# Kernel tuning notes

Hardware: AMD Instinct MI355X
Metric: run time of the kernel (lower is better)

Reference implementation:

```python
import jax, jax.numpy as jnp
import numpy as np

DIM = 1024
NUM_HEADS = 16
HEAD_DIM = DIM // NUM_HEADS


def apply_rotary_embed(x, thetas):
    # x: (..., seq, d), thetas: (seq, d) broadcast over leading dims
    x1, x2 = jnp.split(x, 2, axis=-1)
    x_rot = jnp.concatenate([-x2, x1], axis=-1)
    return x * jnp.cos(thetas) + x_rot * jnp.sin(thetas)


def setup_inputs() -> dict:
    key = jax.random.key(0)
    ks = jax.random.split(key, 8)
    B, Nx, Nc = 4, 1024, 2048
    x = jax.random.normal(ks[0], (B, Nx, DIM), dtype=jnp.float32)
    c = jax.random.normal(ks[1], (B, Nc, DIM), dtype=jnp.float32)
    x_pos_embed = jax.random.normal(ks[2], (Nx, HEAD_DIM), dtype=jnp.float32)
    c_pos_embed = jax.random.normal(ks[3], (Nc, HEAD_DIM), dtype=jnp.float32)
    s = 1.0 / np.sqrt(DIM)
    Wq = jax.random.normal(ks[4], (DIM, DIM), dtype=jnp.float32) * s
    Wkv = jax.random.normal(ks[5], (DIM, 2 * DIM), dtype=jnp.float32) * s
    Wproj = jax.random.normal(ks[6], (DIM, DIM), dtype=jnp.float32) * s
    bproj = jnp.zeros((DIM,), dtype=jnp.float32)
    return {"x": x, "c": c, "x_pos_embed": x_pos_embed, "c_pos_embed": c_pos_embed,
            "Wq": Wq, "Wkv": Wkv, "Wproj": Wproj, "bproj": bproj}


def reference(x, c, x_pos_embed, c_pos_embed, Wq, Wkv, Wproj, bproj):
    B, Nx, D = x.shape
    Nc = c.shape[1]
    H, hd = NUM_HEADS, HEAD_DIM
    # Q projection -> (B, H, Nx, hd)
    q = (x @ Wq).reshape(B, Nx, H, hd).transpose(0, 2, 1, 3)
    q = apply_rotary_embed(q, x_pos_embed)
    # KV projection -> k, v each (B, H, Nc, hd)
    kv = (c @ Wkv).reshape(B, Nc, 2, H, hd).transpose(2, 0, 3, 1, 4)
    k, v = kv[0], kv[1]
    k = apply_rotary_embed(k, c_pos_embed)
    # scaled dot-product attention (dropout p=0 -> identity)
    scale = 1.0 / np.sqrt(hd).astype(np.float32)
    attn = jnp.einsum('bhqd,bhkd->bhqk', q, k) * scale
    attn = jax.nn.softmax(attn, axis=-1)
    out = jnp.einsum('bhqk,bhkd->bhqd', attn, v)
    out = out.transpose(0, 2, 1, 3).reshape(B, Nx, D)
    return out @ Wproj + bproj
```

## Files before the change

kernel.cpp:

```cpp
#include <hip/hip_runtime.h>
#include <math.h>

#define DIMC  1024
#define NHEAD 16
#define HD    64
#define NB    4
#define NX    1024
#define NC    2048
#define KD    1024

typedef _Float16 half_t;
typedef __attribute__((ext_vector_type(8))) _Float16 h8;
typedef __attribute__((ext_vector_type(4))) _Float16 h4;
typedef __attribute__((ext_vector_type(2))) __fp16 fp16x2;
typedef __attribute__((ext_vector_type(4))) float f32x4;

#define QSCALE 0.1803368801111244f
#define NEGM  -8.656170245333781f

__device__ __forceinline__ void gload_lds16(const half_t* g, half_t* l) {
    __builtin_amdgcn_global_load_lds(
        (__attribute__((address_space(1))) void*)(g),
        (__attribute__((address_space(3))) void*)(l), 16, 0, 0);
}

__device__ __forceinline__ void wtile(const float* __restrict__ W,
                                      half_t* __restrict__ Wt, int N, int IMG,
                                      int bx, int by, int t)
{
    __shared__ half_t T[64][72];
    const int k0 = by * 64, n0 = bx * 64;
    const int kr = t >> 2, c0 = (t & 3) << 4;
    const float* src = W + (size_t)(k0 + kr) * N + n0 + c0;
#pragma unroll
    for (int j = 0; j < 16; j += 4) {
        float4 v = *(const float4*)(src + j);
        T[c0 + j + 0][kr] = (half_t)v.x;
        T[c0 + j + 1][kr] = (half_t)v.y;
        T[c0 + j + 2][kr] = (half_t)v.z;
        T[c0 + j + 3][kr] = (half_t)v.w;
    }
    __syncthreads();
    const int nr = t >> 2, kc = (t & 3) << 4;
    if (!IMG) {
        half_t* dst = Wt + (size_t)(n0 + nr) * KD + k0 + kc;
        *(int4*)dst       = *(const int4*)&T[nr][kc];
        *(int4*)(dst + 8) = *(const int4*)&T[nr][kc + 8];
    } else {
        const int n = n0 + nr;
        const int ntile = n >> 8, rr = n & 255;
        const int s0 = kc >> 3;
        half_t* base = Wt + ((size_t)(ntile * 16 + by) * 256 + rr) * 64;
        *(int4*)(base + ((s0 ^ (rr & 7)) << 3))       = *(const int4*)&T[nr][kc];
        *(int4*)(base + (((s0 + 1) ^ (rr & 7)) << 3)) = *(const int4*)&T[nr][kc + 8];
    }
}

__global__ __launch_bounds__(256) void prep(
    const float* __restrict__ x, half_t* __restrict__ xh,
    const float* __restrict__ c, half_t* __restrict__ ch,
    const float* __restrict__ xpe, const float* __restrict__ cpe,
    float* __restrict__ xct, float* __restrict__ xst,
    float* __restrict__ cct, float* __restrict__ cst,
    const float* __restrict__ Wq,  half_t* __restrict__ Wqt,
    const float* __restrict__ Wkv, half_t* __restrict__ Wkt,
    const float* __restrict__ Wp,  half_t* __restrict__ Wpt)
{
    const int bid = blockIdx.x, t = threadIdx.x;
    if (bid < 1024) {
        if (bid < 256)      wtile(Wq,  Wqt, DIMC, 0,     bid & 15,         bid >> 4,         t);
        else if (bid < 768) wtile(Wkv, Wkt, 2 * DIMC, 1, (bid - 256) & 31, (bid - 256) >> 5, t);
        else                wtile(Wp,  Wpt, DIMC, 0,     (bid - 768) & 15, (bid - 768) >> 4, t);
    } else if (bid < 7168) {
        const int nx = NB * NX * DIMC;
        const int i = ((bid - 1024) * 256 + t) * 8;
        const float* s;
        h8 o;
        if (i < nx) {
            s = x + i;
            float4 a = *(const float4*)(s);
            float4 b = *(const float4*)(s + 4);
            o[0] = (half_t)a.x; o[1] = (half_t)a.y; o[2] = (half_t)a.z; o[3] = (half_t)a.w;
            o[4] = (half_t)b.x; o[5] = (half_t)b.y; o[6] = (half_t)b.z; o[7] = (half_t)b.w;
            *(h8*)(xh + i) = o;
        } else {
            const int j = i - nx;
            s = c + j;
            float4 a = *(const float4*)(s);
            float4 b = *(const float4*)(s + 4);
            o[0] = (half_t)a.x; o[1] = (half_t)a.y; o[2] = (half_t)a.z; o[3] = (half_t)a.w;
            o[4] = (half_t)b.x; o[5] = (half_t)b.y; o[6] = (half_t)b.z; o[7] = (half_t)b.w;
            const int R = j >> 10, k = j & 1023;
            const int mt = R >> 8, r = R & 255, kt = k >> 6, sl = (k & 63) >> 3;
            *(h8*)(ch + ((size_t)(mt * 16 + kt) * 256 + r) * 64 + ((sl ^ (r & 7)) << 3)) = o;
        }
    } else {
        const int i = (bid - 7168) * 256 + t;
        if (i < NX * HD) {
            const float th = xpe[i];
            xct[i] = cosf(th); xst[i] = sinf(th);
        } else {
            const int j = i - NX * HD;
            const float th = cpe[j];
            cct[j] = cosf(th); cst[j] = sinf(th);
        }
    }
}

template <int MODE, int BN>
__global__ __launch_bounds__(256) void hgemm(
    const half_t* __restrict__ Ag, const half_t* __restrict__ Bt,
    const float* __restrict__ ct, const float* __restrict__ st,
    const float* __restrict__ bias,
    void* __restrict__ out0, void* __restrict__ out1)
{
    constexpr int MI = (BN == 128) ? 4 : 2;
    constexpr int BLOADS = BN / 32;
    __shared__ half_t As[2][8192];
    __shared__ half_t Bs[2][BN * 64];

    const int tid = threadIdx.x;
    const int w = tid >> 6, lane = tid & 63;
    const int lr = lane & 15, lg = lane >> 4;
    const int wrOff = (BN == 128) ? (w >> 1) * 64 : w * 32;
    const int wcOff = (BN == 128) ? (w & 1) * 64 : 0;

    int lin = (int)blockIdx.x;
    lin = (lin & 7) * ((int)gridDim.x >> 3) + (lin >> 3);
    const int m0 = (lin >> 4) * 128, n0 = (lin & 15) * BN;

    f32x4 acc[MI][4];
#pragma unroll
    for (int i = 0; i < MI; ++i)
#pragma unroll
        for (int j = 0; j < 4; ++j) acc[i][j] = f32x4{0.f, 0.f, 0.f, 0.f};

    size_t gA[4], gB[BLOADS];
    int loff[4];
#pragma unroll
    for (int c = 0; c < 4; ++c) {
        const int L = c * 4096 + w * 1024 + lane * 16;
        const int row = L >> 7;
        const int ss = ((L >> 4) & 7) ^ (row & 7);
        gA[c] = (size_t)(m0 + row) * KD + ss * 8;
        if (c < BLOADS) gB[c] = (size_t)(n0 + row) * KD + ss * 8;
        loff[c] = c * 2048 + w * 512;
    }

#define HSTAGE(buf, kk) do {                                               \
        _Pragma("unroll")                                                  \
        for (int c = 0; c < 4; ++c) {                                      \
            gload_lds16(Ag + gA[c] + (kk) * 64, &As[buf][loff[c]]);        \
            if (c < BLOADS) gload_lds16(Bt + gB[c] + (kk) * 64, &Bs[buf][loff[c]]); \
        }                                                                  \
    } while (0)

    HSTAGE(0, 0);
    asm volatile("s_waitcnt vmcnt(0)" ::: "memory");
    __builtin_amdgcn_s_barrier();
    __builtin_amdgcn_sched_barrier(0);

    for (int k = 0; k < KD / 64; ++k) {
        const int cb = k & 1;
        if (k + 1 < KD / 64) {
            HSTAGE(cb ^ 1, k + 1);
            if constexpr (BLOADS == 4)
                asm volatile("s_waitcnt vmcnt(8)" ::: "memory");
            else
                asm volatile("s_waitcnt vmcnt(6)" ::: "memory");
        } else {
            asm volatile("s_waitcnt vmcnt(0)" ::: "memory");
        }
        __builtin_amdgcn_s_barrier();
        __builtin_amdgcn_sched_barrier(0);

        __builtin_amdgcn_s_setprio(1);
#pragma unroll
        for (int kc = 0; kc < 2; ++kc) {
            h8 af[MI], bf[4];
#pragma unroll
            for (int mi = 0; mi < MI; ++mi) {
                const int r = wrOff + mi * 16 + lr;
                af[mi] = *(const h8*)&As[cb][r * 64 + (((kc * 4 + lg) ^ (r & 7)) << 3)];
            }
#pragma unroll
            for (int ni = 0; ni < 4; ++ni) {
                const int r = wcOff + ni * 16 + lr;
                bf[ni] = *(const h8*)&Bs[cb][r * 64 + (((kc * 4 + lg) ^ (r & 7)) << 3)];
            }
#pragma unroll
            for (int mi = 0; mi < MI; ++mi)
#pragma unroll
                for (int ni = 0; ni < 4; ++ni)
                    acc[mi][ni] = __builtin_amdgcn_mfma_f32_16x16x32_f16(
                        af[mi], bf[ni], acc[mi][ni], 0, 0, 0);
        }
        __builtin_amdgcn_s_setprio(0);

        __builtin_amdgcn_s_barrier();
        __builtin_amdgcn_sched_barrier(0);
    }
#undef HSTAGE

    if (MODE == 2) {
        float* o = (float*)out0;
#pragma unroll
        for (int ni = 0; ni < 4; ++ni) {
            const int col = n0 + ni * 16 + lr;
            const float bv = bias[col];
#pragma unroll
            for (int mi = 0; mi < MI; ++mi)
#pragma unroll
                for (int r = 0; r < 4; ++r) {
                    const int row = m0 + wrOff + mi * 16 + lg * 4 + r;
                    o[(size_t)row * DIMC + col] = acc[mi][ni][r] + bv;
                }
        }
        return;
    }

    if (MODE == 0) {
        half_t* Qw = (half_t*)out0;
        const int h = n0 >> 6;
#pragma unroll
        for (int mi = 0; mi < MI; ++mi)
#pragma unroll
            for (int r = 0; r < 4; ++r) {
                const int row = m0 + wrOff + mi * 16 + lg * 4 + r;
                const int bb = row >> 10, nn = row & (NX - 1);
                const float* cr = ct + nn * HD;
                const float* sr = st + nn * HD;
                half_t* op = Qw + (((size_t)(bb * NHEAD + h)) * NX + nn) * HD;
#pragma unroll
                for (int ni = 0; ni < 4; ++ni) {
                    const int d = ni * 16 + lr;
                    const float val = acc[mi][ni][r];
                    const float pv  = acc[mi][ni ^ 2][r];
                    op[d] = (half_t)((val * cr[d] + (ni < 2 ? -pv : pv) * sr[d]) * QSCALE);
                }
            }
    }
}

__global__ __launch_bounds__(512, 2) void hgemm_kv(
    const half_t* __restrict__ Aimg, const half_t* __restrict__ Bimg,
    const float* __restrict__ ct, const float* __restrict__ st,
    half_t* __restrict__ Kw, half_t* __restrict__ Vw)
{
    __shared__ half_t lds[65536];

    const int tid = threadIdx.x;
    const int w = tid >> 6, lane = tid & 63;
    const int lr = lane & 15, lg = lane >> 4;
    const int wr = w >> 2, wc = w & 3;
    const int wrOff = wr * 128, wcOff = wc * 64;

    int lin = (int)blockIdx.x;
    lin = (lin & 7) * 32 + (lin >> 3);
    const int mt = lin >> 3, nt = lin & 7;
    const int m0 = mt * 256, n0 = nt * 256;

    const half_t* Ablk = Aimg + (size_t)mt * 262144;
    const half_t* Bblk = Bimg + (size_t)nt * 262144;
    const int so2 = w * 512 + lane * 8;

    f32x4 acc[8][4];
#pragma unroll
    for (int i = 0; i < 8; ++i)
#pragma unroll
        for (int j = 0; j < 4; ++j) acc[i][j] = f32x4{0.f, 0.f, 0.f, 0.f};
    h8 af[2][2];
    h8 bf[4][2];

#define ISSUEH(SRC, DSTOFF) do {                                     \
        gload_lds16((SRC) + so2,        &lds[(DSTOFF) + w * 512]);   \
        gload_lds16((SRC) + 4096 + so2, &lds[(DSTOFF) + 4096 + w * 512]); \
    } while (0)

#define PHASE(MI0, AOFF, BOFF, READBF, STG, GATE) do {               \
        _Pragma("unroll")                                            \
        for (int kc = 0; kc < 2; ++kc)                               \
        _Pragma("unroll")                                            \
        for (int d = 0; d < 2; ++d) {                                \
            const int r_ = wrOff + ((MI0) + d) * 16 + lr;            \
            af[d][kc] = *(const h8*)&lds[(AOFF) + r_ * 64 + (((kc * 4 + lg) ^ (r_ & 7)) << 3)]; \
        }                                                            \
        if (READBF) {                                                \
            _Pragma("unroll")                                        \
            for (int ni = 0; ni < 4; ++ni)                           \
            _Pragma("unroll")                                        \
            for (int kc = 0; kc < 2; ++kc) {                         \
                const int rb = wcOff + ni * 16 + lr;                 \
                bf[ni][kc] = *(const h8*)&lds[(BOFF) + rb * 64 + (((kc * 4 + lg) ^ (rb & 7)) << 3)]; \
            }                                                        \
        }                                                            \
        STG;                                                         \
        __builtin_amdgcn_sched_barrier(0);                           \
        __builtin_amdgcn_s_barrier();                                \
        __builtin_amdgcn_s_setprio(1);                               \
        _Pragma("unroll")                                            \
        for (int d = 0; d < 2; ++d)                                  \
        _Pragma("unroll")                                            \
        for (int ni = 0; ni < 4; ++ni)                               \
        _Pragma("unroll")                                            \
        for (int kc = 0; kc < 2; ++kc)                               \
            acc[(MI0) + d][ni] = __builtin_amdgcn_mfma_f32_16x16x32_f16( \
                af[d][kc], bf[ni][kc], acc[(MI0) + d][ni], 0, 0, 0); \
        __builtin_amdgcn_s_setprio(0);                               \
        GATE;                                                        \
        __builtin_amdgcn_s_barrier();                                \
    } while (0)

#define GATE4 asm volatile("s_waitcnt vmcnt(4)" ::: "memory")
#define GATE0 asm volatile("s_waitcnt vmcnt(0)" ::: "memory")
#define NOG   ((void)0)

    ISSUEH(Ablk, 0);          ISSUEH(Ablk + 8192, 8192);
    ISSUEH(Bblk, 32768);      ISSUEH(Bblk + 8192, 32768 + 8192);
    __builtin_amdgcn_sched_barrier(0);
    ISSUEH(Bblk + 16384, 49152); ISSUEH(Bblk + 16384 + 8192, 49152 + 8192);
    asm volatile("s_waitcnt vmcnt(4)" ::: "memory");
    __builtin_amdgcn_s_barrier();

    for (int i = 0; i < 7; ++i) {
        const half_t* An1 = Ablk + (size_t)(2 * i + 1) * 16384;
        const half_t* An2 = Ablk + (size_t)(2 * i + 2) * 16384;
        const half_t* Bn2 = Bblk + (size_t)(2 * i + 2) * 16384;
        const half_t* Bn3 = Bblk + (size_t)(2 * i + 3) * 16384;
        PHASE(0, 0,     32768, true,  ISSUEH(An1, 16384),               NOG);
        PHASE(2, 0,     32768, false, ISSUEH(An1 + 8192, 16384 + 8192), NOG);
        PHASE(4, 0,     32768, false, ISSUEH(Bn2, 32768),               NOG);
        PHASE(6, 0,     32768, false, ISSUEH(Bn2 + 8192, 32768 + 8192), GATE4);
        PHASE(0, 16384, 49152, true,  ISSUEH(An2, 0),                   NOG);
        PHASE(2, 16384, 49152, false, ISSUEH(An2 + 8192, 8192),         NOG);
        PHASE(4, 16384, 49152, false, ISSUEH(Bn3, 49152),               NOG);
        PHASE(6, 16384, 49152, false, ISSUEH(Bn3 + 8192, 49152 + 8192), GATE4);
    }
    {
        const half_t* A15 = Ablk + (size_t)15 * 16384;
        PHASE(0, 0,     32768, true,  ISSUEH(A15, 16384),               NOG);
        PHASE(2, 0,     32768, false, ISSUEH(A15 + 8192, 16384 + 8192), NOG);
        PHASE(4, 0,     32768, false, NOG,                              NOG);
        PHASE(6, 0,     32768, false, NOG,                              GATE0);
        PHASE(0, 16384, 49152, true,  NOG,                              NOG);
        PHASE(2, 16384, 49152, false, NOG,                              NOG);
        PHASE(4, 16384, 49152, false, NOG,                              NOG);
        PHASE(6, 16384, 49152, false, NOG,                              NOG);
    }
#undef PHASE
#undef ISSUEH
#undef GATE4
#undef GATE0
#undef NOG

    const bool isK = (n0 < DIMC);
    const int h = ((n0 & (DIMC - 1)) >> 6) + wc;
#pragma unroll
    for (int mi = 0; mi < 8; ++mi)
#pragma unroll
        for (int r = 0; r < 4; ++r) {
            const int row = m0 + wrOff + mi * 16 + lg * 4 + r;
            const int bb = row >> 11, nn = row & (NC - 1);
            const int tt = nn >> 6, rr = nn & 63;
            const size_t tbase = ((size_t)(bb * NHEAD + h) * 32 + tt) * 4096;
            const float* cr = ct + nn * HD;
            const float* sr = st + nn * HD;
#pragma unroll
            for (int ni = 0; ni < 4; ++ni) {
                const int d = ni * 16 + lr;
                const float val = acc[mi][ni][r];
                if (isK) {
                    const float pv = acc[mi][ni ^ 2][r];
                    Kw[tbase + rr * 64 + ((((d >> 3) ^ (rr & 7)) << 3) | (d & 7))] =
                        (half_t)(val * cr[d] + (ni < 2 ? -pv : pv) * sr[d]);
                } else {
                    Vw[tbase + d * 64 + ((((rr >> 3) ^ (d & 7)) << 3) | (rr & 7))] =
                        (half_t)val;
                }
            }
        }
}

__global__ __launch_bounds__(256) void attn_mfma(
    const half_t* __restrict__ Q, const half_t* __restrict__ Kg,
    const half_t* __restrict__ Vg,
    float* __restrict__ Opart, float* __restrict__ Lpart)
{
    __shared__ half_t Ks[3][4096];
    __shared__ half_t Vs[3][4096];
    __shared__ half_t Ps[16384];

    const int tid = threadIdx.x;
    const int w = tid >> 6, lane = tid & 63;
    const int lr = lane & 15, lg = lane >> 4;
    const int e7 = lr & 7;

    const int inner = (int)blockIdx.x & 255;
    const int kvh = (int)blockIdx.x >> 8;
    const int sid = (inner & 7) * 32 + (inner >> 3);
    const int bh = sid >> 2;
    const int q0 = (sid & 3) * 256;

    h8 qf0[4], qf1[4];
#pragma unroll
    for (int qb = 0; qb < 4; ++qb) {
        const half_t* qbase =
            Q + ((size_t)bh * NX + q0 + qb * 64 + w * 16 + lr) * HD + lg * 8;
        qf0[qb] = *(const h8*)(qbase);
        qf1[qb] = *(const h8*)(qbase + 32);
    }

    f32x4 acc[4][4];
#pragma unroll
    for (int qb = 0; qb < 4; ++qb)
#pragma unroll
        for (int i = 0; i < 4; ++i) acc[qb][i] = f32x4{0.f, 0.f, 0.f, 0.f};
    f32x4 accl[4];
#pragma unroll
    for (int qb = 0; qb < 4; ++qb) accl[qb] = f32x4{0.f, 0.f, 0.f, 0.f};

    h8 vone;
#pragma unroll
    for (int i = 0; i < 8; ++i) vone[i] = (half_t)(lr == 0 ? 1.0f : 0.0f);

    const half_t* Kt = Kg + (size_t)bh * 32 * 4096;
    const half_t* Vt = Vg + (size_t)bh * 32 * 4096;
    const int so = w * 512 + lane * 8;
    const int t0 = kvh * 16;

#define STAGE(bi, t) do {                                           \
        const half_t* kg_ = Kt + (size_t)(t) * 4096;                \
        const half_t* vg_ = Vt + (size_t)(t) * 4096;                \
        gload_lds16(kg_ + so,        &Ks[bi][w * 512]);             \
        gload_lds16(kg_ + 2048 + so, &Ks[bi][2048 + w * 512]);      \
        gload_lds16(vg_ + so,        &Vs[bi][w * 512]);             \
        gload_lds16(vg_ + 2048 + so, &Vs[bi][2048 + w * 512]);      \
    } while (0)

    STAGE(0, t0);

    const int rowq = w * 16 + lr;

    int cur = 0, nxt = 1;
    for (int i = 0; i < 16; ++i) {
        if (i + 1 < 16) {
            STAGE(nxt, t0 + i + 1);
            asm volatile("s_waitcnt vmcnt(4)" ::: "memory");
        } else {
            asm volatile("s_waitcnt vmcnt(0)" ::: "memory");
        }
        __builtin_amdgcn_s_barrier();
        __builtin_amdgcn_sched_barrier(0);

        h8 kfr[4][2];
#pragma unroll
        for (int cb = 0; cb < 4; ++cb) {
            const int r = cb * 16 + lr;
            kfr[cb][0] = *(const h8*)&Ks[cur][r * 64 + ((lg ^ e7) << 3)];
            kfr[cb][1] = *(const h8*)&Ks[cur][r * 64 + (((4 + lg) ^ e7) << 3)];
        }

#pragma unroll
        for (int qb = 0; qb < 4; ++qb) {
            const int rowp = qb * 64 + rowq;

            f32x4 sc[4];
            __builtin_amdgcn_s_setprio(1);
#pragma unroll
            for (int cb = 0; cb < 4; ++cb) {
                f32x4 a = {NEGM, NEGM, NEGM, NEGM};
                a = __builtin_amdgcn_mfma_f32_16x16x32_f16(kfr[cb][0], qf0[qb], a, 0, 0, 0);
                a = __builtin_amdgcn_mfma_f32_16x16x32_f16(kfr[cb][1], qf1[qb], a, 0, 0, 0);
                sc[cb] = a;
            }
            __builtin_amdgcn_s_setprio(0);

#pragma unroll
            for (int cb = 0; cb < 4; ++cb) {
                fp16x2 a01 = __builtin_amdgcn_cvt_pkrtz(exp2f(sc[cb][0]), exp2f(sc[cb][1]));
                fp16x2 a23 = __builtin_amdgcn_cvt_pkrtz(exp2f(sc[cb][2]), exp2f(sc[cb][3]));
                union { h4 h; uint2 u; } pw;
                pw.u.x = *(unsigned int*)&a01;
                pw.u.y = *(unsigned int*)&a23;
                const int s = cb * 2 + (lg >> 1);
                *(h4*)&Ps[rowp * 64 + ((s ^ e7) << 3) + (lg & 1) * 4] = pw.h;
            }
        }

        h8 pf0q[4], pf1q[4];
#pragma unroll
        for (int qb = 0; qb < 4; ++qb) {
            const int rowp = qb * 64 + rowq;
            pf0q[qb] = *(const h8*)&Ps[rowp * 64 + ((lg ^ e7) << 3)];
            pf1q[qb] = *(const h8*)&Ps[rowp * 64 + (((4 + lg) ^ e7) << 3)];
        }

        __builtin_amdgcn_s_setprio(1);
#pragma unroll
        for (int db = 0; db < 4; ++db) {
            const int rd = db * 16 + lr;
            const h8 vf0 = *(const h8*)&Vs[cur][rd * 64 + ((lg ^ e7) << 3)];
            const h8 vf1 = *(const h8*)&Vs[cur][rd * 64 + (((4 + lg) ^ e7) << 3)];
#pragma unroll
            for (int qb = 0; qb < 4; ++qb) {
                acc[qb][db] = __builtin_amdgcn_mfma_f32_16x16x32_f16(pf0q[qb], vf0, acc[qb][db], 0, 0, 0);
                acc[qb][db] = __builtin_amdgcn_mfma_f32_16x16x32_f16(pf1q[qb], vf1, acc[qb][db], 0, 0, 0);
            }
        }
#pragma unroll
        for (int qb = 0; qb < 4; ++qb) {
            accl[qb] = __builtin_amdgcn_mfma_f32_16x16x32_f16(pf0q[qb], vone, accl[qb], 0, 0, 0);
            accl[qb] = __builtin_amdgcn_mfma_f32_16x16x32_f16(pf1q[qb], vone, accl[qb], 0, 0, 0);
        }
        __builtin_amdgcn_s_setprio(0);

        cur = nxt;
        nxt = (nxt == 2) ? 0 : nxt + 1;
    }
#undef STAGE

#pragma unroll
    for (int qb = 0; qb < 4; ++qb) {
        const int qblk = (q0 >> 6) + qb;
        const int slot = (bh * 16 + qblk) * 2 + kvh;
        float* Po = Opart + (size_t)slot * 4096;
#pragma unroll
        for (int db = 0; db < 4; ++db)
#pragma unroll
            for (int r = 0; r < 4; ++r)
                Po[(w * 16 + lg * 4 + r) * 64 + db * 16 + lr] = acc[qb][db][r];
        if (lr == 0) {
#pragma unroll
            for (int r = 0; r < 4; ++r)
                Lpart[(size_t)slot * 64 + w * 16 + lg * 4 + r] = accl[qb][r];
        }
    }
}

__global__ __launch_bounds__(256) void combine(
    const float* __restrict__ Opart, const float* __restrict__ Lpart,
    half_t* __restrict__ Ow)
{
    const int pidx = blockIdx.x;
    const int bh = pidx >> 4, qblk = pidx & 15;
    const int b = bh >> 4, h = bh & 15;
    const int t = threadIdx.x;
    const int row = t >> 2;
    const int c0 = (t & 3) << 4;

    const float* P0 = Opart + (size_t)(pidx * 2 + 0) * 4096 + row * 64 + c0;
    const float* P1 = Opart + (size_t)(pidx * 2 + 1) * 4096 + row * 64 + c0;
    const float inv = 1.f / (Lpart[(size_t)(pidx * 2 + 0) * 64 + row] +
                             Lpart[(size_t)(pidx * 2 + 1) * 64 + row]);

    half_t* o = Ow + ((size_t)b * NX + qblk * 64 + row) * DIMC + h * 64 + c0;
#pragma unroll
    for (int j = 0; j < 16; j += 8) {
        float4 a0 = *(const float4*)(P0 + j);
        float4 a1 = *(const float4*)(P0 + j + 4);
        float4 b0 = *(const float4*)(P1 + j);
        float4 b1 = *(const float4*)(P1 + j + 4);
        h8 ov;
        ov[0] = (half_t)((a0.x + b0.x) * inv);
        ov[1] = (half_t)((a0.y + b0.y) * inv);
        ov[2] = (half_t)((a0.z + b0.z) * inv);
        ov[3] = (half_t)((a0.w + b0.w) * inv);
        ov[4] = (half_t)((a1.x + b1.x) * inv);
        ov[5] = (half_t)((a1.y + b1.y) * inv);
        ov[6] = (half_t)((a1.z + b1.z) * inv);
        ov[7] = (half_t)((a1.w + b1.w) * inv);
        *(h8*)(o + j) = ov;
    }
}

extern "C" void kernel_launch(void* const* d_in, const int* in_sizes, int n_in,
                              void* d_out, int out_size, void* d_ws, size_t ws_size,
                              hipStream_t stream)
{
    const float* x     = (const float*)d_in[0];
    const float* c     = (const float*)d_in[1];
    const float* xpe   = (const float*)d_in[2];
    const float* cpe   = (const float*)d_in[3];
    const float* Wq    = (const float*)d_in[4];
    const float* Wkv   = (const float*)d_in[5];
    const float* Wproj = (const float*)d_in[6];
    const float* bproj = (const float*)d_in[7];

    char* wsb = (char*)d_ws;
    half_t* xh  = (half_t*)(wsb);
    half_t* ch  = (half_t*)(wsb + ((size_t)8  << 20));
    half_t* Wqt = (half_t*)(wsb + ((size_t)24 << 20));
    half_t* Wkt = (half_t*)(wsb + ((size_t)26 << 20));
    half_t* Kw  = (half_t*)(wsb + ((size_t)32 << 20));
    half_t* Vw  = (half_t*)(wsb + ((size_t)48 << 20));
    half_t* Ow  = (half_t*)(wsb + ((size_t)64 << 20));
    float*  xct = (float*)(wsb + ((size_t)72 << 20));
    float*  xst = (float*)(wsb + ((size_t)72 << 20) + (256u << 10));
    float*  cct = (float*)(wsb + ((size_t)72 << 20) + (512u << 10));
    float*  cst = (float*)(wsb + ((size_t)72 << 20) + (1024u << 10));
    half_t* Wpt = (half_t*)(wsb + ((size_t)74 << 20));
    float*  Lpart = (float*)(wsb + ((size_t)76 << 20));
    float*  Opart = (float*)(wsb);
    half_t* Qw  = (half_t*)d_out;

    prep<<<7936, 256, 0, stream>>>(x, xh, c, ch, xpe, cpe,
                                   xct, xst, cct, cst,
                                   Wq, Wqt, Wkv, Wkt, Wproj, Wpt);

    hgemm<0, 64><<<512, 256, 0, stream>>>(xh, Wqt, xct, xst, nullptr,
                                          Qw, nullptr);
    hgemm_kv<<<256, 512, 0, stream>>>(ch, Wkt, cct, cst, Kw, Vw);
    attn_mfma<<<512, 256, 0, stream>>>(Qw, Kw, Vw, Opart, Lpart);
    combine<<<1024, 256, 0, stream>>>(Opart, Lpart, Ow);
    hgemm<2, 64><<<512, 256, 0, stream>>>(Ow, Wpt, nullptr, nullptr, bproj,
                                          (float*)d_out, nullptr);
}
```

Baseline: 181.6 us.

## Merge Q projection GEMM into the KV GEMM launch with a shared tile layout

```diff
diff --git a/kernel.cpp b/kernel.cpp
--- a/kernel.cpp
+++ b/kernel.cpp
@@ -68,24 +68,25 @@
 {
     const int bid = blockIdx.x, t = threadIdx.x;
     if (bid < 1024) {
-        if (bid < 256)      wtile(Wq,  Wqt, DIMC, 0,     bid & 15,         bid >> 4,         t);
+        if (bid < 256)      wtile(Wq,  Wqt, DIMC, 1,     bid & 15,         bid >> 4,         t);
         else if (bid < 768) wtile(Wkv, Wkt, 2 * DIMC, 1, (bid - 256) & 31, (bid - 256) >> 5, t);
         else                wtile(Wp,  Wpt, DIMC, 0,     (bid - 768) & 15, (bid - 768) >> 4, t);
     } else if (bid < 7168) {
         const int nx = NB * NX * DIMC;
         const int i = ((bid - 1024) * 256 + t) * 8;
-        const float* s;
         h8 o;
         if (i < nx) {
-            s = x + i;
+            const float* s = x + i;
             float4 a = *(const float4*)(s);
             float4 b = *(const float4*)(s + 4);
             o[0] = (half_t)a.x; o[1] = (half_t)a.y; o[2] = (half_t)a.z; o[3] = (half_t)a.w;
             o[4] = (half_t)b.x; o[5] = (half_t)b.y; o[6] = (half_t)b.z; o[7] = (half_t)b.w;
-            *(h8*)(xh + i) = o;
+            const int R = i >> 10, k = i & 1023;
+            const int mt = R >> 8, r = R & 255, kt = k >> 6, sl = (k & 63) >> 3;
+            *(h8*)(xh + ((size_t)(mt * 16 + kt) * 256 + r) * 64 + ((sl ^ (r & 7)) << 3)) = o;
         } else {
             const int j = i - nx;
-            s = c + j;
+            const float* s = c + j;
             float4 a = *(const float4*)(s);
             float4 b = *(const float4*)(s + 4);
             o[0] = (half_t)a.x; o[1] = (half_t)a.y; o[2] = (half_t)a.z; o[3] = (half_t)a.w;
@@ -216,36 +217,15 @@
                     o[(size_t)row * DIMC + col] = acc[mi][ni][r] + bv;
                 }
         }
-        return;
-    }
-
-    if (MODE == 0) {
-        half_t* Qw = (half_t*)out0;
-        const int h = n0 >> 6;
-#pragma unroll
-        for (int mi = 0; mi < MI; ++mi)
-#pragma unroll
-            for (int r = 0; r < 4; ++r) {
-                const int row = m0 + wrOff + mi * 16 + lg * 4 + r;
-                const int bb = row >> 10, nn = row & (NX - 1);
-                const float* cr = ct + nn * HD;
-                const float* sr = st + nn * HD;
-                half_t* op = Qw + (((size_t)(bb * NHEAD + h)) * NX + nn) * HD;
-#pragma unroll
-                for (int ni = 0; ni < 4; ++ni) {
-                    const int d = ni * 16 + lr;
-                    const float val = acc[mi][ni][r];
-                    const float pv  = acc[mi][ni ^ 2][r];
-                    op[d] = (half_t)((val * cr[d] + (ni < 2 ? -pv : pv) * sr[d]) * QSCALE);
-                }
-            }
-    }
-}
-
-__global__ __launch_bounds__(512, 2) void hgemm_kv(
+    }
+}
+
+__global__ __launch_bounds__(512, 2) void hgemm_all(
     const half_t* __restrict__ Aimg, const half_t* __restrict__ Bimg,
-    const float* __restrict__ ct, const float* __restrict__ st,
-    half_t* __restrict__ Kw, half_t* __restrict__ Vw)
+    const half_t* __restrict__ Aq,   const half_t* __restrict__ Bq,
+    const float* __restrict__ cct, const float* __restrict__ cst,
+    const float* __restrict__ xct, const float* __restrict__ xst,
+    half_t* __restrict__ Kw, half_t* __restrict__ Vw, half_t* __restrict__ Qw)
 {
     __shared__ half_t lds[65536];
 
@@ -255,13 +235,25 @@
     const int wr = w >> 2, wc = w & 3;
     const int wrOff = wr * 128, wcOff = wc * 64;
 
-    int lin = (int)blockIdx.x;
-    lin = (lin & 7) * 32 + (lin >> 3);
-    const int mt = lin >> 3, nt = lin & 7;
-    const int m0 = mt * 256, n0 = nt * 256;
-
-    const half_t* Ablk = Aimg + (size_t)mt * 262144;
-    const half_t* Bblk = Bimg + (size_t)nt * 262144;
+    const int bid = (int)blockIdx.x;
+    const bool isQ = bid >= 256;
+    int m0, n0;
+    const half_t* Ablk;
+    const half_t* Bblk;
+    if (!isQ) {
+        int lin = (bid & 7) * 32 + (bid >> 3);
+        const int mt = lin >> 3, nt = lin & 7;
+        m0 = mt * 256; n0 = nt * 256;
+        Ablk = Aimg + (size_t)mt * 262144;
+        Bblk = Bimg + (size_t)nt * 262144;
+    } else {
+        const int q = bid - 256;
+        int lin = (q & 7) * 8 + (q >> 3);
+        const int mt = lin >> 2, nt = lin & 3;
+        m0 = mt * 256; n0 = nt * 256;
+        Ablk = Aq + (size_t)mt * 262144;
+        Bblk = Bq + (size_t)nt * 262144;
+    }
     const int so2 = w * 512 + lane * 8;
 
     f32x4 acc[8][4];
@@ -353,32 +345,53 @@
 #undef GATE0
 #undef NOG
 
-    const bool isK = (n0 < DIMC);
-    const int h = ((n0 & (DIMC - 1)) >> 6) + wc;
-#pragma unroll
-    for (int mi = 0; mi < 8; ++mi)
-#pragma unroll
-        for (int r = 0; r < 4; ++r) {
-            const int row = m0 + wrOff + mi * 16 + lg * 4 + r;
-            const int bb = row >> 11, nn = row & (NC - 1);
-            const int tt = nn >> 6, rr = nn & 63;
-            const size_t tbase = ((size_t)(bb * NHEAD + h) * 32 + tt) * 4096;
-            const float* cr = ct + nn * HD;
-            const float* sr = st + nn * HD;
-#pragma unroll
-            for (int ni = 0; ni < 4; ++ni) {
-                const int d = ni * 16 + lr;
-                const float val = acc[mi][ni][r];
-                if (isK) {
-                    const float pv = acc[mi][ni ^ 2][r];
-                    Kw[tbase + rr * 64 + ((((d >> 3) ^ (rr & 7)) << 3) | (d & 7))] =
-                        (half_t)(val * cr[d] + (ni < 2 ? -pv : pv) * sr[d]);
-                } else {
-                    Vw[tbase + d * 64 + ((((rr >> 3) ^ (d & 7)) << 3) | (rr & 7))] =
-                        (half_t)val;
+    if (!isQ) {
+        const bool isK = (n0 < DIMC);
+        const int h = ((n0 & (DIMC - 1)) >> 6) + wc;
+#pragma unroll
+        for (int mi = 0; mi < 8; ++mi)
+#pragma unroll
+            for (int r = 0; r < 4; ++r) {
+                const int row = m0 + wrOff + mi * 16 + lg * 4 + r;
+                const int bb = row >> 11, nn = row & (NC - 1);
+                const int tt = nn >> 6, rr = nn & 63;
+                const size_t tbase = ((size_t)(bb * NHEAD + h) * 32 + tt) * 4096;
+                const float* cr = cct + nn * HD;
+                const float* sr = cst + nn * HD;
+#pragma unroll
+                for (int ni = 0; ni < 4; ++ni) {
+                    const int d = ni * 16 + lr;
+                    const float val = acc[mi][ni][r];
+                    if (isK) {
+                        const float pv = acc[mi][ni ^ 2][r];
+                        Kw[tbase + rr * 64 + ((((d >> 3) ^ (rr & 7)) << 3) | (d & 7))] =
+                            (half_t)(val * cr[d] + (ni < 2 ? -pv : pv) * sr[d]);
+                    } else {
+                        Vw[tbase + d * 64 + ((((rr >> 3) ^ (d & 7)) << 3) | (rr & 7))] =
+                            (half_t)val;
+                    }
                 }
             }
-        }
+    } else {
+        const int h = (n0 >> 6) + wc;
+#pragma unroll
+        for (int mi = 0; mi < 8; ++mi)
+#pragma unroll
+            for (int r = 0; r < 4; ++r) {
+                const int row = m0 + wrOff + mi * 16 + lg * 4 + r;
+                const int bb = row >> 10, nn = row & (NX - 1);
+                const float* cr = xct + nn * HD;
+                const float* sr = xst + nn * HD;
+                half_t* op = Qw + (((size_t)(bb * NHEAD + h)) * NX + nn) * HD;
+#pragma unroll
+                for (int ni = 0; ni < 4; ++ni) {
+                    const int d = ni * 16 + lr;
+                    const float val = acc[mi][ni][r];
+                    const float pv  = acc[mi][ni ^ 2][r];
+                    op[d] = (half_t)((val * cr[d] + (ni < 2 ? -pv : pv) * sr[d]) * QSCALE);
+                }
+            }
+    }
 }
 
 __global__ __launch_bounds__(256) void attn_mfma(
@@ -607,9 +620,9 @@
                                    xct, xst, cct, cst,
                                    Wq, Wqt, Wkv, Wkt, Wproj, Wpt);
 
-    hgemm<0, 64><<<512, 256, 0, stream>>>(xh, Wqt, xct, xst, nullptr,
-                                          Qw, nullptr);
-    hgemm_kv<<<256, 512, 0, stream>>>(ch, Wkt, cct, cst, Kw, Vw);
+    hgemm_all<<<320, 512, 0, stream>>>(ch, Wkt, xh, Wqt,
+                                       cct, cst, xct, xst,
+                                       Kw, Vw, Qw);
     attn_mfma<<<512, 256, 0, stream>>>(Qw, Kw, Vw, Opart, Lpart);
     combine<<<1024, 256, 0, stream>>>(Opart, Lpart, Ow);
     hgemm<2, 64><<<512, 256, 0, stream>>>(Ow, Wpt, nullptr, nullptr, bproj,
```

After: 175.1 us. -3.6%, faster.
